# Kernel optimization log

Hardware: AMD Instinct MI355X
Metric: run time of the kernel (lower is better)

## Reference

```python
import jax, jax.numpy as jnp
import numpy as np

L = 6; C = 320; K = 9; NCLS = 1000; B = 2; IMG = 224
DILS = tuple(min(i // 4 + 1, 49 // K) for i in range(L))  # max_dilation = 49 // k
LOG10 = float(np.log(10.0))
BN_INV = float(1.0 / np.sqrt(1.0 + 1e-5))  # BatchNorm in eval with mean=0, var=1


def _act(x):
    return jax.nn.relu(x)


def _lorentz_linear(x, W, b, log_s):
    # LorentzLinear: nonlin -> affine -> rescale onto the hyperboloid
    y = _act(x) @ W.T + b
    yn = y[..., 1:]
    time = jax.nn.sigmoid(y[..., :1]) * jnp.exp(log_s) + 1.1
    sc = (time * time - 1.0) / jnp.clip(jnp.sum(yn * yn, -1, keepdims=True), 1e-8)
    return jnp.concatenate([time, yn * jnp.sqrt(sc)], -1)


def _ffn(x, w1, b1, s1, w2, b2, s2):
    # FFN_Lorentz: two LorentzLinear layers + residual
    return _lorentz_linear(_lorentz_linear(x, w1, b1, s1), w2, b2, s2) + x


def _conv_bn(x, w, b, g, bt, stride):
    y = jax.lax.conv_general_dilated(x, w, (stride, stride), ((1, 1), (1, 1)),
                                     dimension_numbers=('NCHW', 'OIHW', 'NCHW'))
    y = y + b[None, :, None, None]
    return y * BN_INV * g[None, :, None, None] + bt[None, :, None, None]


def _expmap0_ch(u):
    # Lorentz expmap0 along the channel axis (channel 0 = time)
    us = u[:, 1:]
    nrm = jnp.sqrt(jnp.clip(jnp.sum(us * us, axis=1, keepdims=True), 1e-8))
    return jnp.concatenate([jnp.cosh(nrm), jnp.sinh(nrm) / nrm * us], axis=1)


def _graph_conv(x4, W, b, s, k, dil):
    # LorentzDyGraphConv2d: dilated dense kNN + MRConv-style aggregation + LorentzLinear
    f = x4[..., 0].transpose(0, 2, 1)  # (B, N, C)
    fs = jax.lax.stop_gradient(f)      # kNN graph built without gradient (as in ViG)
    sq = jnp.sum(fs * fs, -1)
    dist = sq[:, :, None] + sq[:, None, :] - 2.0 * jnp.einsum('bic,bjc->bij', fs, fs)
    _, idx = jax.lax.top_k(-dist, k * dil)
    idx = idx[:, :, ::dil]  # dilated neighbors (B, N, k)
    xj = f[jnp.arange(f.shape[0])[:, None, None], idx]  # gather (B, N, k, C)
    m = jnp.max(xj - f[:, :, None, :], axis=2)           # max-relative aggregation
    y = _lorentz_linear(jnp.concatenate([f, m], -1), W, b, s)  # (B, N, C)
    return y.transpose(0, 2, 1)[..., None]


def _block(x, f1w1, f1b1, f1s1, f1w2, f1b2, f1s2, gw, gb, gs,
           f2w1, f2b1, f2s1, f2w2, f2b2, f2s2,
           fw1, fb1, fs1, fw2, fb2, fs2, dil):
    Bb, Cc, H, W = x.shape
    N = H * W
    x4 = x.reshape(Bb, Cc, N, 1)
    shortcut = x4
    t = x4[..., 0].transpose(0, 2, 1)  # rearrange b c h w -> b (h w) c
    t = _ffn(t, f1w1, f1b1, f1s1, f1w2, f1b2, f1s2)
    x4b = t.reshape(Bb, Cc, N, 1)      # raw reshape, faithful to the source
    g = _graph_conv(x4b, gw, gb, gs, K, dil)
    t = g[..., 0].transpose(0, 2, 1)
    t = _ffn(t, f2w1, f2b1, f2s1, f2w2, f2b2, f2s2)
    x4c = t.reshape(Bb, Cc, N, 1) + shortcut  # raw reshape + residual, faithful
    x = x4c.reshape(Bb, Cc, H, W)
    t = x.transpose(0, 2, 3, 1).reshape(Bb, N, Cc)
    t = _ffn(t, fw1, fb1, fs1, fw2, fb2, fs2)
    return t.reshape(Bb, Cc, H, W)     # raw reshape, faithful


def setup_inputs() -> dict:
    key = jax.random.key(0)
    ks = jax.random.split(key, 16)
    half = C // 2
    d = {}
    d['x'] = jax.random.normal(ks[0], (B, 3, IMG, IMG), jnp.float32)
    d['conv1_w'] = jax.random.normal(ks[1], (half, 3, 3, 3), jnp.float32) * 0.05
    d['conv1_b'] = jnp.zeros((half,), jnp.float32)
    d['bn1_g'] = jnp.ones((half,), jnp.float32)
    d['bn1_b'] = jnp.zeros((half,), jnp.float32)
    d['conv2_w'] = jax.random.normal(ks[2], (C, half, 3, 3), jnp.float32) * 0.01
    d['conv2_b'] = jnp.zeros((C,), jnp.float32)
    d['bn2_g'] = jnp.ones((C,), jnp.float32)
    d['bn2_b'] = jnp.zeros((C,), jnp.float32)
    d['conv3_w'] = jax.random.normal(ks[3], (C, C, 3, 3), jnp.float32) * 0.01
    d['conv3_b'] = jnp.zeros((C,), jnp.float32)
    d['bn3_g'] = jnp.ones((C,), jnp.float32)
    d['bn3_b'] = jnp.zeros((C,), jnp.float32)
    d['pos_embed'] = jax.random.normal(ks[4], (1, C, IMG // 4, IMG // 4), jnp.float32) * 0.02
    for j, n in enumerate(['fc1', 'fc2', 'ffn']):
        k1, k2 = jax.random.split(ks[5 + j])
        d[n + '_w1'] = jax.random.normal(k1, (L, C, C), jnp.float32) * (1.0 / C) ** 0.5
        d[n + '_b1'] = jnp.zeros((L, C), jnp.float32)
        d[n + '_s1'] = jnp.full((L,), LOG10, jnp.float32)
        d[n + '_w2'] = jax.random.normal(k2, (L, C, C), jnp.float32) * (1.0 / C) ** 0.5
        d[n + '_b2'] = jnp.zeros((L, C), jnp.float32)
        d[n + '_s2'] = jnp.full((L,), LOG10, jnp.float32)
    d['gc_w'] = jax.random.normal(ks[8], (L, C, 2 * C), jnp.float32) * (1.0 / (2 * C)) ** 0.5
    d['gc_b'] = jnp.zeros((L, C), jnp.float32)
    d['gc_s'] = jnp.full((L,), LOG10, jnp.float32)
    sp = jax.random.normal(ks[9], (NCLS, C - 1), jnp.float32) * (1.0 / C) ** 0.5
    d['cls_w'] = jnp.concatenate([jnp.sqrt(1.0 + jnp.sum(sp * sp, -1, keepdims=True)), sp], -1)
    d['head_b'] = jnp.zeros((NCLS,), jnp.float32)
    return d


def reference(x, conv1_w, conv1_b, bn1_g, bn1_b, conv2_w, conv2_b, bn2_g, bn2_b,
              conv3_w, conv3_b, bn3_g, bn3_b, pos_embed,
              fc1_w1, fc1_b1, fc1_s1, fc1_w2, fc1_b2, fc1_s2,
              gc_w, gc_b, gc_s,
              fc2_w1, fc2_b1, fc2_s1, fc2_w2, fc2_b2, fc2_s2,
              ffn_w1, ffn_b1, ffn_s1, ffn_w2, ffn_b2, ffn_s2,
              cls_w, head_b):
    h = _act(_conv_bn(x, conv1_w, conv1_b, bn1_g, bn1_b, 2))
    h = _act(_conv_bn(h, conv2_w, conv2_b, bn2_g, bn2_b, 2))
    h = _conv_bn(h, conv3_w, conv3_b, bn3_g, bn3_b, 1)
    h = _expmap0_ch(h + pos_embed)
    for i in range(L):
        h = _block(h,
                   fc1_w1[i], fc1_b1[i], fc1_s1[i], fc1_w2[i], fc1_b2[i], fc1_s2[i],
                   gc_w[i], gc_b[i], gc_s[i],
                   fc2_w1[i], fc2_b1[i], fc2_s1[i], fc2_w2[i], fc2_b2[i], fc2_s2[i],
                   ffn_w1[i], ffn_b1[i], ffn_s1[i], ffn_w2[i], ffn_b2[i], ffn_s2[i],
                   DILS[i])
    pooled = jnp.mean(h, axis=(2, 3))  # adaptive_avg_pool2d(x, 1)
    signs = jnp.concatenate([-jnp.ones((1,), pooled.dtype), jnp.ones((C - 1,), pooled.dtype)])
    # Lorentz_MLP_head: 2 + 2 * cinner(x, cls) + bias
    return 2.0 + 2.0 * ((pooled * signs) @ cls_w.T) + head_b
```

## Files before the change

### kernel.cpp

```cpp
#include <hip/hip_runtime.h>
#include <cstdint>
#include <cstddef>

constexpr int CC = 320;
constexpr int NN = 3136;
constexpr int BB = 2;
constexpr int RR = BB * NN;
constexpr float BN_INV_F = 0.9999950000374997f;

__global__ __launch_bounds__(256) void transpose6(
    const float* __restrict__ w0, const float* __restrict__ w1,
    const float* __restrict__ w2, const float* __restrict__ w3,
    const float* __restrict__ w4, const float* __restrict__ w5,
    float* __restrict__ out) {
  size_t e = (size_t)blockIdx.x * 256 + threadIdx.x;
  const size_t per = (size_t)6 * CC * CC;
  if (e >= 6 * per) return;
  int m = (int)(e / per);
  size_t r = e % per;
  int l = (int)(r / (CC * CC));
  int q = (int)(r % (CC * CC));
  int ci = q / CC, co = q % CC;
  const float* src = (m == 0) ? w0 : (m == 1) ? w1 : (m == 2) ? w2
                   : (m == 3) ? w3 : (m == 4) ? w4 : w5;
  out[e] = src[(size_t)l * CC * CC + (size_t)co * CC + ci];
}

__global__ __launch_bounds__(256) void transpose_gc(const float* __restrict__ w,
                                                    float* __restrict__ out) {
  size_t e = (size_t)blockIdx.x * 256 + threadIdx.x;
  const size_t tot = (size_t)6 * 2 * CC * CC;
  if (e >= tot) return;
  int l = (int)(e / (2 * CC * CC));
  int q = (int)(e % (2 * CC * CC));
  int ci = q / CC, co = q % CC;
  out[e] = w[(size_t)l * CC * 2 * CC + (size_t)co * 2 * CC + ci];
}

__global__ __launch_bounds__(256) void transpose_w1(const float* __restrict__ w,
                                                    float* __restrict__ out) {
  int e = blockIdx.x * 256 + threadIdx.x;
  if (e >= 160 * 27) return;
  int oc = e / 27, k = e % 27;
  out[k * 160 + oc] = w[e];
}

template <int K>
__global__ __launch_bounds__(256) void transpose_conv(const float* __restrict__ w,
                                                      float* __restrict__ out) {
  int e = blockIdx.x * 256 + threadIdx.x;
  if (e >= K * 320) return;
  int k = e / 320, co = e % 320;
  out[e] = w[(size_t)co * K + k];
}

__global__ __launch_bounds__(160) void conv1_kernel(const float* __restrict__ x,
                                                    const float* __restrict__ w1t,
                                                    const float* __restrict__ cb,
                                                    const float* __restrict__ g,
                                                    const float* __restrict__ bt,
                                                    float* __restrict__ C1) {
  int pix = blockIdx.x;
  int oc = threadIdx.x;
  int b = pix / 12544;
  int r = pix % 12544;
  int oh = r / 112, ow = r % 112;
  int ih0 = 2 * oh - 1, iw0 = 2 * ow - 1;
  float acc = 0.f;
#pragma unroll
  for (int ic = 0; ic < 3; ic++) {
    const float* xc = x + ((size_t)(b * 3 + ic)) * 224 * 224;
#pragma unroll
    for (int kh = 0; kh < 3; kh++) {
      int ih = ih0 + kh;
      if (ih < 0 || ih >= 224) continue;
#pragma unroll
      for (int kw = 0; kw < 3; kw++) {
        int iw = iw0 + kw;
        if (iw < 0 || iw >= 224) continue;
        acc = fmaf(xc[(size_t)ih * 224 + iw], w1t[(ic * 9 + kh * 3 + kw) * 160 + oc], acc);
      }
    }
  }
  float y = (acc + cb[oc]) * (BN_INV_F * g[oc]) + bt[oc];
  C1[(size_t)pix * 160 + oc] = fmaxf(y, 0.f);
}

template <int CIN, int IH, int IW, int S>
__global__ __launch_bounds__(256) void im2col_k(const float* __restrict__ src,
                                                float* __restrict__ COL) {
  constexpr int K = CIN * 9;
  int row = blockIdx.x;
  int b = row / 3136, pix = row % 3136;
  int oh = pix / 56, ow = pix % 56;
  int ih0 = S * oh - 1, iw0 = S * ow - 1;
  float* dst = COL + (size_t)row * K;
  for (int k = threadIdx.x; k < K; k += 256) {
    int ic = k / 9;
    int khw = k - ic * 9;
    int kh = khw / 3, kw = khw - kh * 3;
    int ih = ih0 + kh, iw = iw0 + kw;
    float v = 0.f;
    if (ih >= 0 && ih < IH && iw >= 0 && iw < IW)
      v = src[(((size_t)(b * IH + ih)) * IW + iw) * CIN + ic];
    dst[k] = v;
  }
}

__global__ __launch_bounds__(CC) void expmap_tok_kernel(const float* __restrict__ h,
                                                        const float* __restrict__ pos,
                                                        float* __restrict__ X) {
  int bn = blockIdx.x;
  int n = bn % NN;
  int c = threadIdx.x;
  float u = h[(size_t)bn * CC + c] + pos[(size_t)c * NN + n];
  float v = (c == 0) ? 0.f : u * u;
#pragma unroll
  for (int o = 32; o > 0; o >>= 1) v += __shfl_down(v, o, 64);
  __shared__ float red[5];
  __shared__ float fac[2];
  if ((c & 63) == 0) red[c >> 6] = v;
  __syncthreads();
  if (c == 0) {
    float s = red[0] + red[1] + red[2] + red[3] + red[4];
    float nrm = sqrtf(fmaxf(s, 1e-8f));
    fac[0] = coshf(nrm);
    fac[1] = sinhf(nrm) / nrm;
  }
  __syncthreads();
  X[(size_t)bn * CC + c] = (c == 0) ? fac[0] : fac[1] * u;
}

__global__ __launch_bounds__(256) void pperm_kernel(const float* __restrict__ U,
                                                    const float* __restrict__ add,
                                                    float* __restrict__ V) {
  __shared__ float t[64][65];
  int b = blockIdx.z;
  int n0 = blockIdx.x * 64;
  int c0 = blockIdx.y * 64;
  const float* Ub = U + (size_t)b * NN * CC;
  float* Vb = V + (size_t)b * NN * CC;
  const float* Ab = add ? add + (size_t)b * NN * CC : nullptr;
  int tx = threadIdx.x & 63;
  int ty = threadIdx.x >> 6;
#pragma unroll
  for (int i = 0; i < 16; i++) {
    int c = ty * 16 + i;
    t[c][tx] = Ub[(size_t)(c0 + c) * NN + n0 + tx];
  }
  __syncthreads();
#pragma unroll
  for (int i = 0; i < 16; i++) {
    int n = ty * 16 + i;
    float v = t[tx][n];
    size_t o = (size_t)(n0 + n) * CC + c0 + tx;
    if (Ab) v += Ab[o];
    Vb[o] = v;
  }
}

template <bool ARELU, int EPI>
__global__ __launch_bounds__(128) void gemm_t(const float* __restrict__ A,
                                              const float* __restrict__ BW,
                                              const float* __restrict__ bias,
                                              const float* __restrict__ bng,
                                              const float* __restrict__ bnb,
                                              float* __restrict__ C, int M, int K) {
  __shared__ float As[32][68];
  __shared__ float Bs[32][68];
  int tid = threadIdx.x;
  int n0 = blockIdx.x * 64;
  int m0 = blockIdx.y * 64;
  int lm = tid >> 1;
  int lk8 = (tid & 1) * 8;
  int bk = tid >> 4;
  int bn = (tid & 15) << 2;
  int tm = (tid >> 4) << 3;
  int tn = (tid & 15) << 2;
  float acc[8][4] = {};
  float4 ra[4], rb[4];
  const float* aprow = A + (size_t)(m0 + lm) * K + lk8;

  auto load_tile = [&](int k0) {
    const float* ap = aprow + k0;
    ra[0] = *(const float4*)ap;
    ra[1] = *(const float4*)(ap + 4);
    ra[2] = *(const float4*)(ap + 16);
    ra[3] = *(const float4*)(ap + 20);
#pragma unroll
    for (int h = 0; h < 4; h++)
      rb[h] = *(const float4*)(BW + (size_t)(k0 + bk + h * 8) * CC + n0 + bn);
  };
  auto store_tile = [&]() {
#pragma unroll
    for (int h = 0; h < 2; h++) {
      float4 a0 = ra[h * 2], a1 = ra[h * 2 + 1];
      if (ARELU) {
        a0.x = fmaxf(a0.x, 0.f); a0.y = fmaxf(a0.y, 0.f);
        a0.z = fmaxf(a0.z, 0.f); a0.w = fmaxf(a0.w, 0.f);
        a1.x = fmaxf(a1.x, 0.f); a1.y = fmaxf(a1.y, 0.f);
        a1.z = fmaxf(a1.z, 0.f); a1.w = fmaxf(a1.w, 0.f);
      }
      int kb = lk8 + h * 16;
      As[kb + 0][lm] = a0.x; As[kb + 1][lm] = a0.y;
      As[kb + 2][lm] = a0.z; As[kb + 3][lm] = a0.w;
      As[kb + 4][lm] = a1.x; As[kb + 5][lm] = a1.y;
      As[kb + 6][lm] = a1.z; As[kb + 7][lm] = a1.w;
    }
#pragma unroll
    for (int h = 0; h < 4; h++)
      *(float4*)&Bs[bk + h * 8][bn] = rb[h];
  };
  auto compute = [&]() {
#pragma unroll
    for (int k = 0; k < 32; k++) {
      float4 av0 = *(const float4*)&As[k][tm];
      float4 av1 = *(const float4*)&As[k][tm + 4];
      float4 bv = *(const float4*)&Bs[k][tn];
      float aa[8] = {av0.x, av0.y, av0.z, av0.w, av1.x, av1.y, av1.z, av1.w};
      float bb[4] = {bv.x, bv.y, bv.z, bv.w};
#pragma unroll
      for (int i = 0; i < 8; i++)
#pragma unroll
        for (int j = 0; j < 4; j++) acc[i][j] = fmaf(aa[i], bb[j], acc[i][j]);
    }
  };

  load_tile(0);
  store_tile();
  __syncthreads();
  for (int k0 = 32; k0 < K; k0 += 32) {
    load_tile(k0);
    compute();
    __syncthreads();
    store_tile();
    __syncthreads();
  }
  compute();

  float4 bv = *(const float4*)(bias + n0 + tn);
  float bb[4] = {bv.x, bv.y, bv.z, bv.w};
  float gg[4], tt[4];
  if (EPI >= 1) {
    float4 gv = *(const float4*)(bng + n0 + tn);
    float4 tv = *(const float4*)(bnb + n0 + tn);
    gg[0] = gv.x; gg[1] = gv.y; gg[2] = gv.z; gg[3] = gv.w;
    tt[0] = tv.x; tt[1] = tv.y; tt[2] = tv.z; tt[3] = tv.w;
  }
#pragma unroll
  for (int i = 0; i < 8; i++) {
    float o[4];
#pragma unroll
    for (int j = 0; j < 4; j++) {
      float y = acc[i][j] + bb[j];
      if (EPI >= 1) y = y * (BN_INV_F * gg[j]) + tt[j];
      if (EPI == 2) y = fmaxf(y, 0.f);
      o[j] = y;
    }
    float4 ov = {o[0], o[1], o[2], o[3]};
    *(float4*)(C + (size_t)(m0 + tm + i) * CC + n0 + tn) = ov;
  }
}

__global__ __launch_bounds__(256) void lorentz_norm(const float* __restrict__ Y,
                                                    const float* __restrict__ logs, int l,
                                                    const float* __restrict__ res1,
                                                    float* __restrict__ out) {
  int lane = threadIdx.x & 63;
  size_t row = (size_t)blockIdx.x * 4 + (threadIdx.x >> 6);
  const float* y = Y + row * CC;
  float v[5];
  float ss = 0.f;
#pragma unroll
  for (int q = 0; q < 5; q++) {
    v[q] = y[q * 64 + lane];
    float z = v[q] * v[q];
    if (q == 0 && lane == 0) z = 0.f;
    ss += z;
  }
#pragma unroll
  for (int o = 32; o > 0; o >>= 1) ss += __shfl_down(ss, o, 64);
  ss = __shfl(ss, 0, 64);
  float y0 = __shfl(v[0], 0, 64);
  float scale = expf(logs[l]);
  float tmv = scale / (1.f + expf(-y0)) + 1.1f;
  float rf = sqrtf((tmv * tmv - 1.f) / fmaxf(ss, 1e-8f));
#pragma unroll
  for (int q = 0; q < 5; q++) {
    int c = q * 64 + lane;
    float o = (c == 0) ? tmv : v[q] * rf;
    if (res1) o += res1[row * CC + c];
    out[row * CC + c] = o;
  }
}

__global__ __launch_bounds__(256) void sq_kernel(const float* __restrict__ Y,
                                                 float* __restrict__ sq) {
  int lane = threadIdx.x & 63;
  size_t row = (size_t)blockIdx.x * 4 + (threadIdx.x >> 6);
  const float* y = Y + row * CC;
  float ss = 0.f;
#pragma unroll
  for (int q = 0; q < 5; q++) {
    float v = y[q * 64 + lane];
    ss += v * v;
  }
#pragma unroll
  for (int o = 32; o > 0; o >>= 1) ss += __shfl_down(ss, o, 64);
  if (lane == 0) sq[row] = ss;
}

__global__ __launch_bounds__(128) void dist_gemm(const float* __restrict__ Y,
                                                 const float* __restrict__ sq,
                                                 float* __restrict__ D) {
  __shared__ float As[32][68];
  __shared__ float Bs[32][68];
  int tid = threadIdx.x;
  int j0 = blockIdx.x * 64;
  int i0 = blockIdx.y * 64;
  int lm = tid >> 1;
  int lk8 = (tid & 1) * 8;
  int tm = (tid >> 4) << 3;
  int tn = (tid & 15) << 2;
  float acc[8][4] = {};
  float4 ra[4], rb[4];
  const float* aprow = Y + (size_t)(i0 + lm) * CC + lk8;
  const float* bprow = Y + (size_t)(j0 + lm) * CC + lk8;

  auto load_tile = [&](int k0) {
    const float* ap = aprow + k0;
    ra[0] = *(const float4*)ap;
    ra[1] = *(const float4*)(ap + 4);
    ra[2] = *(const float4*)(ap + 16);
    ra[3] = *(const float4*)(ap + 20);
    const float* bp = bprow + k0;
    rb[0] = *(const float4*)bp;
    rb[1] = *(const float4*)(bp + 4);
    rb[2] = *(const float4*)(bp + 16);
    rb[3] = *(const float4*)(bp + 20);
  };
  auto store_tile = [&]() {
#pragma unroll
    for (int h = 0; h < 2; h++) {
      int kb = lk8 + h * 16;
      float4 a0 = ra[h * 2], a1 = ra[h * 2 + 1];
      As[kb + 0][lm] = a0.x; As[kb + 1][lm] = a0.y;
      As[kb + 2][lm] = a0.z; As[kb + 3][lm] = a0.w;
      As[kb + 4][lm] = a1.x; As[kb + 5][lm] = a1.y;
      As[kb + 6][lm] = a1.z; As[kb + 7][lm] = a1.w;
      float4 b0 = rb[h * 2], b1 = rb[h * 2 + 1];
      Bs[kb + 0][lm] = b0.x; Bs[kb + 1][lm] = b0.y;
      Bs[kb + 2][lm] = b0.z; Bs[kb + 3][lm] = b0.w;
      Bs[kb + 4][lm] = b1.x; Bs[kb + 5][lm] = b1.y;
      Bs[kb + 6][lm] = b1.z; Bs[kb + 7][lm] = b1.w;
    }
  };
  auto compute = [&]() {
#pragma unroll
    for (int k = 0; k < 32; k++) {
      float4 av0 = *(const float4*)&As[k][tm];
      float4 av1 = *(const float4*)&As[k][tm + 4];
      float4 bv = *(const float4*)&Bs[k][tn];
      float aa[8] = {av0.x, av0.y, av0.z, av0.w, av1.x, av1.y, av1.z, av1.w};
      float bb[4] = {bv.x, bv.y, bv.z, bv.w};
#pragma unroll
      for (int i = 0; i < 8; i++)
#pragma unroll
        for (int j = 0; j < 4; j++) acc[i][j] = fmaf(aa[i], bb[j], acc[i][j]);
    }
  };

  load_tile(0);
  store_tile();
  __syncthreads();
  for (int k0 = 32; k0 < CC; k0 += 32) {
    load_tile(k0);
    compute();
    __syncthreads();
    store_tile();
    __syncthreads();
  }
  compute();

  float sqi[8], sqj[4];
#pragma unroll
  for (int i = 0; i < 8; i++) sqi[i] = sq[i0 + tm + i];
#pragma unroll
  for (int j = 0; j < 4; j++) sqj[j] = sq[j0 + tn + j];
#pragma unroll
  for (int i = 0; i < 8; i++) {
    float4 o;
    o.x = sqi[i] + sqj[0] - 2.f * acc[i][0];
    o.y = sqi[i] + sqj[1] - 2.f * acc[i][1];
    o.z = sqi[i] + sqj[2] - 2.f * acc[i][2];
    o.w = sqi[i] + sqj[3] - 2.f * acc[i][3];
    *(float4*)(D + (size_t)(i0 + tm + i) * NN + j0 + tn) = o;
  }
}

template <int KT, int DIL>
__global__ __launch_bounds__(256) void topk_kernel(const float* __restrict__ D,
                                                   int* __restrict__ idxout) {
  int lane = threadIdx.x & 63;
  int row = blockIdx.x * 4 + (threadIdx.x >> 6);
  const float* d = D + (size_t)row * NN;
  float ld[KT];
  int li[KT];
#pragma unroll
  for (int q = 0; q < KT; q++) { ld[q] = 3.4e38f; li[q] = 0x7FFFFFFF; }
  for (int t = 0; t < NN / 64; t++) {
    int j = t * 64 + lane;
    float x = d[j];
    if (x < ld[KT - 1]) {
      ld[KT - 1] = x;
      li[KT - 1] = j;
#pragma unroll
      for (int p = KT - 1; p > 0; p--) {
        if (ld[p] < ld[p - 1]) {
          float tf = ld[p]; ld[p] = ld[p - 1]; ld[p - 1] = tf;
          int ti = li[p]; li[p] = li[p - 1]; li[p - 1] = ti;
        }
      }
    }
  }
#pragma unroll 1
  for (int q = 0; q < KT; q++) {
    float bd = ld[0];
    int bi = li[0];
#pragma unroll
    for (int s = 32; s > 0; s >>= 1) {
      float od = __shfl_xor(bd, s, 64);
      int oi = __shfl_xor(bi, s, 64);
      if (od < bd || (od == bd && oi < bi)) { bd = od; bi = oi; }
    }
    if (ld[0] == bd && li[0] == bi) {
#pragma unroll
      for (int p = 0; p < KT - 1; p++) { ld[p] = ld[p + 1]; li[p] = li[p + 1]; }
      ld[KT - 1] = 3.4e38f;
      li[KT - 1] = 0x7FFFFFFF;
    }
    if (lane == 0 && (q % DIL) == 0) idxout[(size_t)row * 9 + q / DIL] = bi;
  }
}

__global__ __launch_bounds__(CC) void gather_max_cat(const float* __restrict__ Y,
                                                     const int* __restrict__ idx,
                                                     float* __restrict__ cat) {
  int bn = blockIdx.x;
  int c = threadIdx.x;
  int b = bn / NN;
  float yc = Y[(size_t)bn * CC + c];
  const int* ip = idx + (size_t)bn * 9;
  float mx = -3.4e38f;
#pragma unroll
  for (int q = 0; q < 9; q++) {
    int j = ip[q];
    mx = fmaxf(mx, Y[((size_t)b * NN + j) * CC + c]);
  }
  cat[(size_t)bn * 2 * CC + c] = yc;
  cat[(size_t)bn * 2 * CC + CC + c] = mx - yc;
}

__global__ __launch_bounds__(CC) void pool_kernel(const float* __restrict__ X,
                                                  float* __restrict__ pooled) {
  int b = blockIdx.y;
  int chunk = blockIdx.x;
  int c = threadIdx.x;
  const float* p = X + ((size_t)b * NN + (size_t)chunk * 64) * CC + c;
  float s = 0.f;
#pragma unroll
  for (int q = 0; q < 64; q++) s += p[(size_t)q * CC];
  atomicAdd(&pooled[b * CC + c], s);
}

__global__ __launch_bounds__(256) void head_kernel(const float* __restrict__ pooled,
                                                   const float* __restrict__ clsw,
                                                   const float* __restrict__ hb,
                                                   float* __restrict__ out) {
  int t = blockIdx.x * 256 + threadIdx.x;
  if (t >= BB * 1000) return;
  int b = t / 1000, k = t % 1000;
  const float* pw = pooled + b * CC;
  const float* cw = clsw + (size_t)k * CC;
  float acc = 0.f;
  for (int c = 0; c < CC; c++) {
    float sgn = (c == 0) ? -1.f : 1.f;
    acc = fmaf(pw[c] * sgn, cw[c], acc);
  }
  out[t] = 2.f + 2.f * (acc * (1.f / 3136.f)) + hb[k];
}

extern "C" void kernel_launch(void* const* d_in, const int* in_sizes, int n_in,
                              void* d_out, int out_size, void* d_ws, size_t ws_size,
                              hipStream_t stream) {
  const float* x = (const float*)d_in[0];
  const float* c1w = (const float*)d_in[1];
  const float* c1b = (const float*)d_in[2];
  const float* bn1g = (const float*)d_in[3];
  const float* bn1b = (const float*)d_in[4];
  const float* c2w = (const float*)d_in[5];
  const float* c2b = (const float*)d_in[6];
  const float* bn2g = (const float*)d_in[7];
  const float* bn2b = (const float*)d_in[8];
  const float* c3w = (const float*)d_in[9];
  const float* c3b = (const float*)d_in[10];
  const float* bn3g = (const float*)d_in[11];
  const float* bn3b = (const float*)d_in[12];
  const float* pos = (const float*)d_in[13];
  const float* fc1w1 = (const float*)d_in[14];
  const float* fc1b1 = (const float*)d_in[15];
  const float* fc1s1 = (const float*)d_in[16];
  const float* fc1w2 = (const float*)d_in[17];
  const float* fc1b2 = (const float*)d_in[18];
  const float* fc1s2 = (const float*)d_in[19];
  const float* fc2w1 = (const float*)d_in[20];
  const float* fc2b1 = (const float*)d_in[21];
  const float* fc2s1 = (const float*)d_in[22];
  const float* fc2w2 = (const float*)d_in[23];
  const float* fc2b2 = (const float*)d_in[24];
  const float* fc2s2 = (const float*)d_in[25];
  const float* ffnw1 = (const float*)d_in[26];
  const float* ffnb1 = (const float*)d_in[27];
  const float* ffns1 = (const float*)d_in[28];
  const float* ffnw2 = (const float*)d_in[29];
  const float* ffnb2 = (const float*)d_in[30];
  const float* ffns2 = (const float*)d_in[31];
  const float* gcw = (const float*)d_in[32];
  const float* gcb = (const float*)d_in[33];
  const float* gcs = (const float*)d_in[34];
  const float* clsw = (const float*)d_in[35];
  const float* headb = (const float*)d_in[36];
  float* out = (float*)d_out;

  float* ws = (float*)d_ws;
  size_t off = 0;
  auto alloc = [&](size_t n) { float* p = ws + off; off += n; return p; };
  float* WT6 = alloc((size_t)6 * 6 * CC * CC);
  float* GCT = alloc((size_t)6 * 2 * CC * CC);
  float* W1T = alloc(27 * 160);
  float* C1 = alloc((size_t)BB * 112 * 112 * 160);
  float* C2 = alloc((size_t)RR * CC);
  float* C3 = alloc((size_t)RR * CC);
  float* X  = alloc((size_t)RR * CC);
  float* T1 = alloc((size_t)RR * CC);
  float* TMP = alloc((size_t)RR * CC);
  float* T2 = alloc((size_t)RR * CC);
  float* F  = alloc((size_t)RR * CC);
  float* Y  = alloc((size_t)RR * CC);
  float* T4 = alloc((size_t)RR * CC);
  float* T5 = alloc((size_t)RR * CC);
  float* T6 = alloc((size_t)RR * CC);
  float* CAT = alloc((size_t)RR * 2 * CC);
  float* COL = T1;
  float* WT2 = COL + (size_t)RR * 2880;
  float* WT3 = WT2 + (size_t)1440 * 320;
  float* DIST = alloc((size_t)NN * NN);
  float* SQ = alloc(RR);
  float* POOL = alloc(BB * CC);
  int* IDX = (int*)(ws + off);
  off += (size_t)RR * 9;

  {
    size_t tot = (size_t)6 * 6 * CC * CC;
    transpose6<<<dim3((unsigned)((tot + 255) / 256)), 256, 0, stream>>>(
        fc1w1, fc1w2, fc2w1, fc2w2, ffnw1, ffnw2, WT6);
    size_t tg = (size_t)6 * 2 * CC * CC;
    transpose_gc<<<dim3((unsigned)((tg + 255) / 256)), 256, 0, stream>>>(gcw, GCT);
    transpose_w1<<<dim3((160 * 27 + 255) / 256), 256, 0, stream>>>(c1w, W1T);
    transpose_conv<1440><<<dim3((1440 * 320 + 255) / 256), 256, 0, stream>>>(c2w, WT2);
    transpose_conv<2880><<<dim3((2880 * 320 + 255) / 256), 256, 0, stream>>>(c3w, WT3);
  }

  dim3 ggrid(5, 98);

  conv1_kernel<<<dim3(BB * 112 * 112), 160, 0, stream>>>(x, W1T, c1b, bn1g, bn1b, C1);
  im2col_k<160, 112, 112, 2><<<dim3(RR), 256, 0, stream>>>(C1, COL);
  gemm_t<false, 2><<<ggrid, 128, 0, stream>>>(COL, WT2, c2b, bn2g, bn2b, C2, RR, 1440);
  im2col_k<320, 56, 56, 1><<<dim3(RR), 256, 0, stream>>>(C2, COL);
  gemm_t<false, 1><<<ggrid, 128, 0, stream>>>(COL, WT3, c3b, bn3g, bn3b, C3, RR, 2880);
  expmap_tok_kernel<<<dim3(RR), CC, 0, stream>>>(C3, pos, X);

  dim3 pgrid(49, 5, BB);
  for (int l = 0; l < 6; l++) {
    const float* w11 = WT6 + ((size_t)0 * 6 + l) * CC * CC;
    const float* w12 = WT6 + ((size_t)1 * 6 + l) * CC * CC;
    const float* w21 = WT6 + ((size_t)2 * 6 + l) * CC * CC;
    const float* w22 = WT6 + ((size_t)3 * 6 + l) * CC * CC;
    const float* wf1 = WT6 + ((size_t)4 * 6 + l) * CC * CC;
    const float* wf2 = WT6 + ((size_t)5 * 6 + l) * CC * CC;
    const float* wgc = GCT + (size_t)l * 2 * CC * CC;

    gemm_t<true, 0><<<ggrid, 128, 0, stream>>>(X, w11, fc1b1 + l * CC, nullptr, nullptr, TMP, RR, CC);
    lorentz_norm<<<RR / 4, 256, 0, stream>>>(TMP, fc1s1, l, nullptr, T1);
    gemm_t<true, 0><<<ggrid, 128, 0, stream>>>(T1, w12, fc1b2 + l * CC, nullptr, nullptr, TMP, RR, CC);
    lorentz_norm<<<RR / 4, 256, 0, stream>>>(TMP, fc1s2, l, X, T2);

    pperm_kernel<<<pgrid, 256, 0, stream>>>(T2, nullptr, F);

    sq_kernel<<<RR / 4, 256, 0, stream>>>(F, SQ);
    for (int b = 0; b < BB; b++) {
      dist_gemm<<<dim3(49, 49), 128, 0, stream>>>(F + (size_t)b * NN * CC, SQ + (size_t)b * NN, DIST);
      if (l < 4)
        topk_kernel<9, 1><<<NN / 4, 256, 0, stream>>>(DIST, IDX + (size_t)b * NN * 9);
      else
        topk_kernel<18, 2><<<NN / 4, 256, 0, stream>>>(DIST, IDX + (size_t)b * NN * 9);
    }
    gather_max_cat<<<RR, CC, 0, stream>>>(F, IDX, CAT);
    gemm_t<true, 0><<<ggrid, 128, 0, stream>>>(CAT, wgc, gcb + l * CC, nullptr, nullptr, TMP, RR, 2 * CC);
    lorentz_norm<<<RR / 4, 256, 0, stream>>>(TMP, gcs, l, nullptr, Y);

    gemm_t<true, 0><<<ggrid, 128, 0, stream>>>(Y, w21, fc2b1 + l * CC, nullptr, nullptr, TMP, RR, CC);
    lorentz_norm<<<RR / 4, 256, 0, stream>>>(TMP, fc2s1, l, nullptr, T1);
    gemm_t<true, 0><<<ggrid, 128, 0, stream>>>(T1, w22, fc2b2 + l * CC, nullptr, nullptr, TMP, RR, CC);
    lorentz_norm<<<RR / 4, 256, 0, stream>>>(TMP, fc2s2, l, Y, T4);

    pperm_kernel<<<pgrid, 256, 0, stream>>>(T4, X, T5);

    gemm_t<true, 0><<<ggrid, 128, 0, stream>>>(T5, wf1, ffnb1 + l * CC, nullptr, nullptr, TMP, RR, CC);
    lorentz_norm<<<RR / 4, 256, 0, stream>>>(TMP, ffns1, l, nullptr, T1);
    gemm_t<true, 0><<<ggrid, 128, 0, stream>>>(T1, wf2, ffnb2 + l * CC, nullptr, nullptr, TMP, RR, CC);
    lorentz_norm<<<RR / 4, 256, 0, stream>>>(TMP, ffns2, l, T5, T6);

    pperm_kernel<<<pgrid, 256, 0, stream>>>(T6, nullptr, X);
  }

  hipMemsetAsync(POOL, 0, (size_t)BB * CC * sizeof(float), stream);
  pool_kernel<<<dim3(49, BB), CC, 0, stream>>>(X, POOL);
  head_kernel<<<dim3((BB * 1000 + 255) / 256), 256, 0, stream>>>(POOL, clsw, headb, out);
}
```

Baseline: 4.482 ms.

## Fuse Lorentz normalization prologue into following linear GEMM

Adds a gemm_nrm kernel that loads a full 32-row strip of the pre-norm activations into shared memory, applies the Lorentz rescale and ReLU in place, then runs the 320-wide GEMM against it. Four separate lorentz_norm launches per layer are replaced, which removes the write and re-read of normalized intermediates. The normalization is recomputed redundantly by each of the 5 column blocks, and one block writes Y when it is needed for the residual. The fused kernel uses smaller 32x64 tiles and a large shared-memory footprint, which may reduce occupancy compared with the original GEMM.

```diff
diff --git a/kernel.cpp b/kernel.cpp
--- a/kernel.cpp
+++ b/kernel.cpp
@@ -258,6 +258,115 @@
       o[j] = y;
     }
     float4 ov = {o[0], o[1], o[2], o[3]};
+    *(float4*)(C + (size_t)(m0 + tm + i) * CC + n0 + tn) = ov;
+  }
+}
+
+__global__ __launch_bounds__(128) void gemm_nrm(const float* __restrict__ A,
+                                                const float* __restrict__ BW,
+                                                const float* __restrict__ bias,
+                                                const float* __restrict__ logs, int l,
+                                                float* __restrict__ wbY,
+                                                float* __restrict__ C) {
+  __shared__ float As[32][324];
+  __shared__ float Bs[32][68];
+  int tid = threadIdx.x;
+  int n0 = blockIdx.x * 64;
+  int m0 = blockIdx.y * 32;
+  for (int f = tid; f < 2560; f += 128) {
+    int row = f / 80;
+    int c4 = (f - row * 80) * 4;
+    float4 a = *(const float4*)(A + (size_t)(m0 + row) * CC + c4);
+    As[row][c4] = a.x; As[row][c4 + 1] = a.y;
+    As[row][c4 + 2] = a.z; As[row][c4 + 3] = a.w;
+  }
+  __syncthreads();
+  {
+    int wave = tid >> 6, lane = tid & 63;
+    float scale = expf(logs[l]);
+    bool wb = (wbY != nullptr) && (blockIdx.x == 0);
+    for (int r = 0; r < 16; r++) {
+      int row = wave * 16 + r;
+      float v[5];
+      float ss = 0.f;
+#pragma unroll
+      for (int q = 0; q < 5; q++) {
+        v[q] = As[row][q * 64 + lane];
+        float z = v[q] * v[q];
+        if (q == 0 && lane == 0) z = 0.f;
+        ss += z;
+      }
+#pragma unroll
+      for (int o = 32; o > 0; o >>= 1) ss += __shfl_down(ss, o, 64);
+      ss = __shfl(ss, 0, 64);
+      float y0 = __shfl(v[0], 0, 64);
+      float tmv = scale / (1.f + expf(-y0)) + 1.1f;
+      float rf = sqrtf((tmv * tmv - 1.f) / fmaxf(ss, 1e-8f));
+#pragma unroll
+      for (int q = 0; q < 5; q++) {
+        int c = q * 64 + lane;
+        float o2 = (c == 0) ? tmv : v[q] * rf;
+        if (wb) wbY[(size_t)(m0 + row) * CC + c] = o2;
+        As[row][c] = fmaxf(o2, 0.f);
+      }
+    }
+  }
+  __syncthreads();
+  int bk = tid >> 4;
+  int bn = (tid & 15) << 2;
+  int tm = (tid >> 4) << 2;
+  int tn = (tid & 15) << 2;
+  float acc[4][4] = {};
+  float4 rb[4];
+  auto loadB = [&](int k0) {
+#pragma unroll
+    for (int h = 0; h < 4; h++)
+      rb[h] = *(const float4*)(BW + (size_t)(k0 + bk + h * 8) * CC + n0 + bn);
+  };
+  auto storeB = [&]() {
+#pragma unroll
+    for (int h = 0; h < 4; h++)
+      *(float4*)&Bs[bk + h * 8][bn] = rb[h];
+  };
+  auto compute = [&](int kbase) {
+#pragma unroll
+    for (int kk = 0; kk < 32; kk += 4) {
+      float av[4][4];
+#pragma unroll
+      for (int i = 0; i < 4; i++) {
+        float4 t = *(const float4*)&As[tm + i][kbase + kk];
+        av[i][0] = t.x; av[i][1] = t.y; av[i][2] = t.z; av[i][3] = t.w;
+      }
+#pragma unroll
+      for (int kq = 0; kq < 4; kq++) {
+        float4 bv = *(const float4*)&Bs[kk + kq][tn];
+        float bb[4] = {bv.x, bv.y, bv.z, bv.w};
+#pragma unroll
+        for (int i = 0; i < 4; i++)
+#pragma unroll
+          for (int j = 0; j < 4; j++)
+            acc[i][j] = fmaf(av[i][kq], bb[j], acc[i][j]);
+      }
+    }
+  };
+  loadB(0);
+  storeB();
+  __syncthreads();
+  for (int k0 = 32; k0 < CC; k0 += 32) {
+    loadB(k0);
+    compute(k0 - 32);
+    __syncthreads();
+    storeB();
+    __syncthreads();
+  }
+  compute(CC - 32);
+  float4 bv = *(const float4*)(bias + n0 + tn);
+  float bb[4] = {bv.x, bv.y, bv.z, bv.w};
+#pragma unroll
+  for (int i = 0; i < 4; i++) {
+    float4 ov;
+    ov.x = acc[i][0] + bb[0]; ov.y = acc[i][1] + bb[1];
+    ov.z = acc[i][2] + bb[2]; ov.w = acc[i][3] + bb[3];
     *(float4*)(C + (size_t)(m0 + tm + i) * CC + n0 + tn) = ov;
   }
 }
@@ -572,6 +681,7 @@
   }
 
   dim3 ggrid(5, 98);
+  dim3 ngrid(5, 196);
 
   conv1_kernel<<<dim3(BB * 112 * 112), 160, 0, stream>>>(x, W1T, c1b, bn1g, bn1b, C1);
   im2col_k<160, 112, 112, 2><<<dim3(RR), 256, 0, stream>>>(C1, COL);
@@ -591,9 +701,8 @@
     const float* wgc = GCT + (size_t)l * 2 * CC * CC;
 
     gemm_t<true, 0><<<ggrid, 128, 0, stream>>>(X, w11, fc1b1 + l * CC, nullptr, nullptr, TMP, RR, CC);
-    lorentz_norm<<<RR / 4, 256, 0, stream>>>(TMP, fc1s1, l, nullptr, T1);
-    gemm_t<true, 0><<<ggrid, 128, 0, stream>>>(T1, w12, fc1b2 + l * CC, nullptr, nullptr, TMP, RR, CC);
-    lorentz_norm<<<RR / 4, 256, 0, stream>>>(TMP, fc1s2, l, X, T2);
+    gemm_nrm<<<ngrid, 128, 0, stream>>>(TMP, w12, fc1b2 + l * CC, fc1s1, l, nullptr, T1);
+    lorentz_norm<<<RR / 4, 256, 0, stream>>>(T1, fc1s2, l, X, T2);
 
     pperm_kernel<<<pgrid, 256, 0, stream>>>(T2, nullptr, F);
 
@@ -607,19 +716,15 @@
     }
     gather_max_cat<<<RR, CC, 0, stream>>>(F, IDX, CAT);
     gemm_t<true, 0><<<ggrid, 128, 0, stream>>>(CAT, wgc, gcb + l * CC, nullptr, nullptr, TMP, RR, 2 * CC);
-    lorentz_norm<<<RR / 4, 256, 0, stream>>>(TMP, gcs, l, nullptr, Y);
-
-    gemm_t<true, 0><<<ggrid, 128, 0, stream>>>(Y, w21, fc2b1 + l * CC, nullptr, nullptr, TMP, RR, CC);
-    lorentz_norm<<<RR / 4, 256, 0, stream>>>(TMP, fc2s1, l, nullptr, T1);
-    gemm_t<true, 0><<<ggrid, 128, 0, stream>>>(T1, w22, fc2b2 + l * CC, nullptr, nullptr, TMP, RR, CC);
+    gemm_nrm<<<ngrid, 128, 0, stream>>>(TMP, w21, fc2b1 + l * CC, gcs, l, Y, T1);
+    gemm_nrm<<<ngrid, 128, 0, stream>>>(T1, w22, fc2b2 + l * CC, fc2s1, l, nullptr, TMP);
     lorentz_norm<<<RR / 4, 256, 0, stream>>>(TMP, fc2s2, l, Y, T4);
 
     pperm_kernel<<<pgrid, 256, 0, stream>>>(T4, X, T5);
 
     gemm_t<true, 0><<<ggrid, 128, 0, stream>>>(T5, wf1, ffnb1 + l * CC, nullptr, nullptr, TMP, RR, CC);
-    lorentz_norm<<<RR / 4, 256, 0, stream>>>(TMP, ffns1, l, nullptr, T1);
-    gemm_t<true, 0><<<ggrid, 128, 0, stream>>>(T1, wf2, ffnb2 + l * CC, nullptr, nullptr, TMP, RR, CC);
-    lorentz_norm<<<RR / 4, 256, 0, stream>>>(TMP, ffns2, l, T5, T6);
+    gemm_nrm<<<ngrid, 128, 0, stream>>>(TMP, wf2, ffnb2 + l * CC, ffns1, l, nullptr, T1);
+    lorentz_norm<<<RR / 4, 256, 0, stream>>>(T1, ffns2, l, T5, T6);
 
     pperm_kernel<<<pgrid, 256, 0, stream>>>(T6, nullptr, X);
   }
```

New measurement: 4.941 ms. 10.3% more time.
